# Performance work log

Measured on AMD Instinct MI355X. Metric: run time of the kernel, lower is better.

The kernel has to match this reference:

```python
import jax, jax.numpy as jnp
import numpy as np

POS_TH = 0.5
NEG_TH = 0.4
NEGPOS_RATIO = 3
BBOX_ALPHA = 1.5
CONF_ALPHA = 1.0
VAR_CXCY = 0.1
VAR_WH = 0.2
NUM_CLASSES = 41
B, P, G = 8, 100000, 16


def setup_inputs() -> dict:
    key = jax.random.key(0)
    k = jax.random.split(key, 8)
    loc_data = jax.random.normal(k[0], (B, P, 4), dtype=jnp.float32)
    conf_data = jax.random.normal(k[1], (B, P, NUM_CLASSES), dtype=jnp.float32)
    # priors in (cx, cy, w, h), normalized coords
    p_cxy = jax.random.uniform(k[2], (P, 2), minval=0.0, maxval=1.0)
    p_wh = jax.random.uniform(k[3], (P, 2), minval=0.02, maxval=0.3)
    priors = jnp.concatenate([p_cxy, p_wh], axis=1).astype(jnp.float32)
    # gt boxes in point form (x1, y1, x2, y2)
    g_cxy = jax.random.uniform(k[4], (B, G, 2), minval=0.15, maxval=0.85)
    g_wh = jax.random.uniform(k[5], (B, G, 2), minval=0.05, maxval=0.4)
    gt_boxes = jnp.concatenate([
        jnp.clip(g_cxy - g_wh / 2, 0.0, 1.0),
        jnp.clip(g_cxy + g_wh / 2, 0.0, 1.0),
    ], axis=-1).astype(jnp.float32)
    gt_labels = jax.random.randint(k[6], (B, G), 1, NUM_CLASSES)
    return {"loc_data": loc_data, "conf_data": conf_data, "priors": priors,
            "gt_boxes": gt_boxes, "gt_labels": gt_labels}


def point_form(pr):
    return jnp.concatenate([pr[:, :2] - pr[:, 2:] / 2,
                            pr[:, :2] + pr[:, 2:] / 2], axis=1)


def jaccard(a, b):
    # a: [G,4] xyxy, b: [P,4] xyxy -> [G,P]
    lt = jnp.maximum(a[:, None, :2], b[None, :, :2])
    rb = jnp.minimum(a[:, None, 2:], b[None, :, 2:])
    wh = jnp.clip(rb - lt, 0.0)
    inter = wh[..., 0] * wh[..., 1]
    area_a = ((a[:, 2] - a[:, 0]) * (a[:, 3] - a[:, 1]))[:, None]
    area_b = ((b[:, 2] - b[:, 0]) * (b[:, 3] - b[:, 1]))[None, :]
    return inter / (area_a + area_b - inter)


def encode(matched, priors):
    # matched [P,4] xyxy, priors [P,4] cxcywh -> SSD offsets with variances
    g_cxcy = ((matched[:, :2] + matched[:, 2:]) / 2 - priors[:, :2]) / (VAR_CXCY * priors[:, 2:])
    g_wh = jnp.log(jnp.clip((matched[:, 2:] - matched[:, :2]) / priors[:, 2:], 1e-8)) / VAR_WH
    return jnp.concatenate([g_cxcy, g_wh], axis=1)


def match_one(gt_box, gt_label, priors):
    # gt_box [G,4], gt_label [G], priors [P,4] -> loc_t [P,4], conf_t [P]
    pf = point_form(priors)
    ov = jaccard(gt_box, pf)                      # [G,P]
    best_truth_ov = ov.max(axis=0)                # [P]
    best_truth_idx = ov.argmax(axis=0)            # [P]
    best_prior_idx = ov.argmax(axis=1)            # [G] best prior per gt
    # force-match each gt to its best prior
    best_truth_ov = best_truth_ov.at[best_prior_idx].set(2.0)
    best_truth_idx = best_truth_idx.at[best_prior_idx].set(jnp.arange(gt_box.shape[0]))
    conf = gt_label[best_truth_idx]
    conf = jnp.where(best_truth_ov < POS_TH, -1, conf)   # neutral
    conf = jnp.where(best_truth_ov < NEG_TH, 0, conf)    # background
    loc = encode(gt_box[best_truth_idx], priors)
    return loc, conf


def reference(loc_data, conf_data, priors, gt_boxes, gt_labels):
    bsz, n_pri, n_cls = conf_data.shape
    loc_t, conf_t = jax.vmap(match_one, in_axes=(0, 0, None))(gt_boxes, gt_labels, priors)
    pos = conf_t > 0                               # [B,P]
    num_pos = pos.sum(axis=1)                      # [B]
    # pos_weights: uniform 1/num_pos per image (ones split then normalized)
    pos_w = pos.astype(loc_data.dtype) / jnp.clip(num_pos, 1).astype(loc_data.dtype)[:, None]
    # localization: weighted SmoothL1 over positives
    d = loc_data - loc_t
    sl1 = jnp.where(jnp.abs(d) < 1.0, 0.5 * d * d, jnp.abs(d) - 0.5)
    loss_B = (pos_w[..., None] * sl1).sum() * BBOX_ALPHA
    # OHEM hard negative mining on background-suppression loss
    loss_c = jax.nn.logsumexp(conf_data, axis=-1) - conf_data[..., 0]
    loss_c = jnp.where(pos | (conf_t < 0), 0.0, loss_c)
    order = jnp.argsort(-loss_c, axis=1)
    rank = jnp.argsort(order, axis=1)
    num_neg = jnp.clip(NEGPOS_RATIO * num_pos, 0, n_pri - 1)
    neg = (rank < num_neg[:, None]) & (~pos) & (conf_t >= 0)
    keep = (pos | neg).astype(conf_data.dtype)
    logp = jax.nn.log_softmax(conf_data, axis=-1)
    ce = -jnp.take_along_axis(logp, jnp.clip(conf_t, 0)[..., None], axis=-1)[..., 0]
    total_pos = jnp.clip(num_pos.sum(), 1).astype(conf_data.dtype)
    loss_C = (ce * keep).sum() * CONF_ALPHA / total_pos
    return (loss_B + loss_C) / bsz
```

## Files before the change

### kernel.cpp

```cpp
#include <hip/hip_runtime.h>
#include <stdint.h>

#define BATCH 8
#define NPRI 100000
#define NGT 16
#define NCLS 41
#define F_POS_TH 0.5f
#define F_NEG_TH 0.4f

static constexpr int TPB = 256;
static constexpr int PBLK = (NPRI + TPB - 1) / TPB;
static constexpr int HBLK = 64;
static constexpr int NBIN = 4096;

static constexpr size_t OFF_KEY  = 0;
static constexpr size_t OFF_CE   = OFF_KEY + (size_t)BATCH*NPRI*8;
static constexpr size_t OFF_CT   = OFF_CE  + (size_t)BATCH*NPRI*4;
static constexpr size_t OFF_OV   = OFF_CT  + (size_t)BATCH*NPRI*4;
static constexpr size_t OFF_BTI  = OFF_OV  + (size_t)BATCH*NPRI*4;
static constexpr size_t OFF_GTC  = OFF_BTI + (size_t)BATCH*NPRI*4;
static constexpr size_t OFF_ZERO = OFF_GTC + BATCH*NGT*8;
static constexpr size_t OFF_HIST = OFF_ZERO;
static constexpr size_t OFF_PREF = OFF_HIST + (size_t)4*BATCH*NBIN*4;
static constexpr size_t OFF_KREM = OFF_PREF + BATCH*8;
static constexpr size_t OFF_NPOS = OFF_KREM + BATCH*4;
static constexpr size_t OFF_SL1  = OFF_NPOS + BATCH*4;
static constexpr size_t OFF_CES  = OFF_SL1  + BATCH*4;
static constexpr size_t ZERO_BYTES = OFF_CES + BATCH*4 - OFF_ZERO;

__device__ inline float smoothl1(float d) {
  float a = fabsf(d);
  return a < 1.f ? 0.5f * d * d : a - 0.5f;
}

__global__ void k_init(unsigned long long* __restrict__ gtc) {
  int i = threadIdx.x;
  if (i < BATCH * NGT) gtc[i] = 0xFFFFFFFFull;
}

__global__ __launch_bounds__(TPB) void k_match(const float* __restrict__ priors,
                                               const float* __restrict__ gtb,
                                               float* __restrict__ ov_out,
                                               int* __restrict__ bti_out,
                                               unsigned long long* __restrict__ gtc) {
  int b = blockIdx.y;
  int t = threadIdx.x;
  int p = blockIdx.x * TPB + t;
  __shared__ unsigned long long best[NGT];
  if (t < NGT) best[t] = 0;
  __syncthreads();
  bool valid = p < NPRI;
  int pc = valid ? p : 0;
  const float4 pv = ((const float4*)priors)[pc];
  float px1 = pv.x - 0.5f * pv.z, py1 = pv.y - 0.5f * pv.w;
  float px2 = pv.x + 0.5f * pv.z, py2 = pv.y + 0.5f * pv.w;
  float parea = (px2 - px1) * (py2 - py1);
  float bov = 0.f; int bidx = 0;
#pragma unroll
  for (int g = 0; g < NGT; g++) {
    const float4 gv = ((const float4*)gtb)[b * NGT + g];
    float ix = fmaxf(fminf(px2, gv.z) - fmaxf(px1, gv.x), 0.f);
    float iy = fmaxf(fminf(py2, gv.w) - fmaxf(py1, gv.y), 0.f);
    float inter = ix * iy;
    float garea = (gv.z - gv.x) * (gv.w - gv.y);
    float iou = inter / (parea + garea - inter);
    if (!valid) iou = 0.f;
    if (iou > bov) { bov = iou; bidx = g; }
    if (iou > 0.f) {
      unsigned long long comp = ((unsigned long long)__float_as_uint(iou) << 32)
                              | (unsigned long long)(0xFFFFFFFFu - (unsigned)p);
      if (comp > best[g]) atomicMax(&best[g], comp);
    }
  }
  if (valid) {
    ov_out[b * NPRI + p] = bov;
    bti_out[b * NPRI + p] = bidx;
  }
  __syncthreads();
  if (t < NGT && best[t] != 0) atomicMax(&gtc[b * NGT + t], best[t]);
}

__global__ __launch_bounds__(TPB) void k_conf(
    const float* __restrict__ loc, const float* __restrict__ conf,
    const float* __restrict__ priors, const float* __restrict__ gtb,
    const int* __restrict__ gtl, const unsigned long long* __restrict__ gtc,
    const float* __restrict__ ov, const int* __restrict__ bti,
    unsigned long long* __restrict__ key, float* __restrict__ ce,
    int* __restrict__ ct, unsigned* __restrict__ npos, float* __restrict__ sl1sum) {
  __shared__ float rows[TPB * NCLS];
  __shared__ float red_s[4];
  __shared__ unsigned red_p[4];
  int b = blockIdx.y;
  int p0 = blockIdx.x * TPB;
  int t = threadIdx.x;
  int nrows = min(TPB, NPRI - p0);
  int n4 = nrows * NCLS / 4;
  const float4* src4 = (const float4*)(conf + ((size_t)b * NPRI + p0) * NCLS);
  float4* rows4 = (float4*)rows;
  if (nrows == TPB) {
    float4 tmp[10];
#pragma unroll
    for (int u = 0; u < 10; u++) tmp[u] = src4[t + u * TPB];
    float4 extra = src4[10 * TPB + t];
#pragma unroll
    for (int u = 0; u < 10; u++) rows4[t + u * TPB] = tmp[u];
    if (t < n4 - 10 * TPB) rows4[10 * TPB + t] = extra;
  } else {
    for (int i = t; i < n4; i += TPB) rows4[i] = src4[i];
  }
  __syncthreads();
  int p = p0 + t;
  bool valid = p < NPRI;
  float my_sl1 = 0.f;
  unsigned my_pos = 0;
  if (valid) {
    float o = ov[b * NPRI + p];
    int g = bti[b * NPRI + p];
#pragma unroll
    for (int gg = 0; gg < NGT; gg++) {
      unsigned long long c64 = gtc[b * NGT + gg];
      unsigned pw = 0xFFFFFFFFu - (unsigned)(c64 & 0xFFFFFFFFull);
      if ((unsigned)p == pw) { o = 2.0f; g = gg; }
    }
    int c = gtl[b * NGT + g];
    if (o < F_POS_TH) c = -1;
    if (o < F_NEG_TH) c = 0;
    ct[b * NPRI + p] = c;
    const float* r = rows + t * NCLS;
    float s = 0.f;
#pragma unroll
    for (int j = 0; j < NCLS; j++) s += __expf(r[j]);
    float lse = __logf(s);
    int tgt = c > 0 ? c : 0;
    ce[b * NPRI + p] = lse - r[tgt];
    float lc = (c == 0) ? (lse - r[0]) : 0.f;
    key[b * NPRI + p] = ((unsigned long long)__float_as_uint(lc) << 17)
                      | (unsigned long long)(0x1FFFFu - (unsigned)p);
    if (c > 0) {
      my_pos = 1;
      const float4 pv = ((const float4*)priors)[p];
      const float4 gv = ((const float4*)gtb)[b * NGT + g];
      float tx = ((gv.x + gv.z) * 0.5f - pv.x) / (0.1f * pv.z);
      float ty = ((gv.y + gv.w) * 0.5f - pv.y) / (0.1f * pv.w);
      float tw = __logf(fmaxf((gv.z - gv.x) / pv.z, 1e-8f)) / 0.2f;
      float th = __logf(fmaxf((gv.w - gv.y) / pv.w, 1e-8f)) / 0.2f;
      const float4 ld = ((const float4*)loc)[(size_t)b * NPRI + p];
      my_sl1 = smoothl1(ld.x - tx) + smoothl1(ld.y - ty)
             + smoothl1(ld.z - tw) + smoothl1(ld.w - th);
    }
  }
  float vs = my_sl1; unsigned vp = my_pos;
#pragma unroll
  for (int off = 32; off; off >>= 1) {
    vs += __shfl_down(vs, off, 64);
    vp += __shfl_down(vp, off, 64);
  }
  if ((t & 63) == 0) { red_s[t >> 6] = vs; red_p[t >> 6] = vp; }
  __syncthreads();
  if (t == 0) {
    float ts = red_s[0] + red_s[1] + red_s[2] + red_s[3];
    unsigned tp = red_p[0] + red_p[1] + red_p[2] + red_p[3];
    if (tp) atomicAdd(&npos[b], tp);
    if (ts != 0.f) atomicAdd(&sl1sum[b], ts);
  }
}

__global__ __launch_bounds__(TPB) void k_histp(const unsigned long long* __restrict__ key,
                                               unsigned* __restrict__ hist,
                                               const unsigned long long* __restrict__ prefix,
                                               int shift) {
  __shared__ unsigned h[NBIN];
  int b = blockIdx.y;
  int t = threadIdx.x;
  for (int i = t; i < NBIN; i += TPB) h[i] = 0;
  __syncthreads();
  unsigned long long pre = prefix[b] >> (shift + 12);
  for (int i = blockIdx.x * TPB + t; i < NPRI; i += HBLK * TPB) {
    unsigned long long k = key[b * NPRI + i];
    if ((k >> (shift + 12)) == pre)
      atomicAdd(&h[(unsigned)((k >> shift) & 0xFFFull)], 1u);
  }
  __syncthreads();
  for (int i = t; i < NBIN; i += TPB) {
    unsigned v = h[i];
    if (v) atomicAdd(&hist[((size_t)b << 12) + i], v);
  }
}

__global__ __launch_bounds__(256) void k_fine(const unsigned* __restrict__ hist,
                                              unsigned long long* __restrict__ prefix,
                                              unsigned* __restrict__ krem,
                                              const unsigned* __restrict__ npos,
                                              int shift, int pass) {
  int b = blockIdx.x;
  int t = threadIdx.x;
  __shared__ unsigned part[256];
  __shared__ unsigned suf[256];
  __shared__ int wA;
  __shared__ unsigned kexclA;
  unsigned k = (pass == 0) ? min(3u * npos[b], (unsigned)(NPRI - 1)) : krem[b];
  if (k == 0) {
    if (t == 0) prefix[b] = ~0ull;
    return;
  }
  const unsigned* h = hist + ((size_t)b << 12);
  unsigned s = 0;
#pragma unroll
  for (int u = 0; u < 16; u++) s += h[t * 16 + u];
  part[t] = s; suf[t] = s;
  __syncthreads();
  for (int off = 1; off < 256; off <<= 1) {
    unsigned v = (t + off < 256) ? suf[t + off] : 0;
    __syncthreads();
    suf[t] += v;
    __syncthreads();
  }
  unsigned excl = suf[t] - part[t];
  if (excl < k && k <= excl + part[t]) { wA = t; kexclA = excl; }
  __syncthreads();
  int w = wA;
  unsigned exclw = kexclA;
  if (t < 64) {
    unsigned v = (t < 16) ? h[w * 16 + t] : 0;
    unsigned sufv = v;
#pragma unroll
    for (int off = 1; off < 16; off <<= 1) {
      unsigned x = __shfl_down(sufv, off, 64);
      if (t + off < 16) sufv += x;
    }
    unsigned excl2 = exclw + (sufv - v);
    if (t < 16 && excl2 < k && k <= excl2 + v) {
      unsigned digit = (unsigned)(w * 16 + t);
      prefix[b] |= ((unsigned long long)digit) << shift;
      krem[b] = k - excl2;
    }
  }
}

__global__ __launch_bounds__(TPB) void k_eval(const unsigned long long* __restrict__ key,
                                              const float* __restrict__ ce,
                                              const int* __restrict__ ct,
                                              const unsigned long long* __restrict__ prefix,
                                              float* __restrict__ cesum) {
  __shared__ float red[4];
  int b = blockIdx.y;
  int t = threadIdx.x;
  int p = blockIdx.x * TPB + t;
  float v = 0.f;
  if (p < NPRI) {
    int c = ct[b * NPRI + p];
    bool keep = (c > 0) || (c == 0 && key[b * NPRI + p] >= prefix[b]);
    if (keep) v = ce[b * NPRI + p];
  }
#pragma unroll
  for (int off = 32; off; off >>= 1) v += __shfl_down(v, off, 64);
  if ((t & 63) == 0) red[t >> 6] = v;
  __syncthreads();
  if (t == 0) {
    float tv = red[0] + red[1] + red[2] + red[3];
    if (tv != 0.f) atomicAdd(&cesum[b], tv);
  }
}

__global__ void k_final(const float* __restrict__ sl1sum, const unsigned* __restrict__ npos,
                        const float* __restrict__ cesum, float* __restrict__ out) {
  if (threadIdx.x == 0 && blockIdx.x == 0) {
    float lb = 0.f, cs = 0.f;
    unsigned tp = 0;
    for (int b = 0; b < BATCH; b++) {
      lb += sl1sum[b] / fmaxf((float)npos[b], 1.f);
      tp += npos[b];
      cs += cesum[b];
    }
    float lc = cs / fmaxf((float)tp, 1.f);
    out[0] = (1.5f * lb + 1.0f * lc) / (float)BATCH;
  }
}

extern "C" void kernel_launch(void* const* d_in, const int* in_sizes, int n_in,
                              void* d_out, int out_size, void* d_ws, size_t ws_size,
                              hipStream_t stream) {
  const float* loc = (const float*)d_in[0];
  const float* conf = (const float*)d_in[1];
  const float* priors = (const float*)d_in[2];
  const float* gtb = (const float*)d_in[3];
  const int* gtl = (const int*)d_in[4];
  char* ws = (char*)d_ws;
  unsigned long long* key = (unsigned long long*)(ws + OFF_KEY);
  float* ce = (float*)(ws + OFF_CE);
  int* ct = (int*)(ws + OFF_CT);
  float* ov = (float*)(ws + OFF_OV);
  int* bti = (int*)(ws + OFF_BTI);
  unsigned long long* gtc = (unsigned long long*)(ws + OFF_GTC);
  unsigned* hist = (unsigned*)(ws + OFF_HIST);
  unsigned long long* prefix = (unsigned long long*)(ws + OFF_PREF);
  unsigned* krem = (unsigned*)(ws + OFF_KREM);
  unsigned* npos = (unsigned*)(ws + OFF_NPOS);
  float* sl1sum = (float*)(ws + OFF_SL1);
  float* cesum = (float*)(ws + OFF_CES);
  float* out = (float*)d_out;

  hipMemsetAsync(ws + OFF_ZERO, 0, ZERO_BYTES, stream);
  k_init<<<1, 128, 0, stream>>>(gtc);
  dim3 gridP(PBLK, BATCH);
  k_match<<<gridP, TPB, 0, stream>>>(priors, gtb, ov, bti, gtc);
  k_conf<<<gridP, TPB, 0, stream>>>(loc, conf, priors, gtb, gtl, gtc, ov, bti,
                                    key, ce, ct, npos, sl1sum);
  dim3 gridH(HBLK, BATCH);
  const int shifts[4] = {36, 24, 12, 0};
  for (int pass = 0; pass < 4; pass++) {
    unsigned* h = hist + (size_t)pass * BATCH * NBIN;
    k_histp<<<gridH, TPB, 0, stream>>>(key, h, prefix, shifts[pass]);
    k_fine<<<BATCH, 256, 0, stream>>>(h, prefix, krem, npos, shifts[pass], pass);
  }
  k_eval<<<gridP, TPB, 0, stream>>>(key, ce, ct, prefix, cesum);
  k_final<<<1, 64, 0, stream>>>(sl1sum, npos, cesum, out);
}
```

Before: 182.0 us.

## Fuse radix-select histogram and scan via last-block ticket, sum negatives from histograms

Merges the per-pass histogram and prefix-select kernels into one kernel. The last block to finish, detected with an atomic ticket, performs the scan and resets the global histograms. Each bin now also accumulates the sum of its keys' loss values, so the hard-negative CE sum comes straight from the histograms and the separate eval pass plus the ce/ct buffers go away. The final reduction moves into the last pass, and k_conf now reads conf rows directly per thread rather than staging them through shared memory. The trade-offs are float-atomic summation order, a ticket-based cross-block sync, uncoalesced strided row reads in k_conf, and a tie at the threshold handled by proportional averaging.

After: 344.2 us. 89.1% more time.

```diff
diff --git a/kernel.cpp b/kernel.cpp
--- a/kernel.cpp
+++ b/kernel.cpp
@@ -14,28 +14,42 @@
 static constexpr int NBIN = 4096;
 
 static constexpr size_t OFF_KEY  = 0;
-static constexpr size_t OFF_CE   = OFF_KEY + (size_t)BATCH*NPRI*8;
-static constexpr size_t OFF_CT   = OFF_CE  + (size_t)BATCH*NPRI*4;
-static constexpr size_t OFF_OV   = OFF_CT  + (size_t)BATCH*NPRI*4;
+static constexpr size_t OFF_OV   = OFF_KEY + (size_t)BATCH*NPRI*8;
 static constexpr size_t OFF_BTI  = OFF_OV  + (size_t)BATCH*NPRI*4;
 static constexpr size_t OFF_GTC  = OFF_BTI + (size_t)BATCH*NPRI*4;
 static constexpr size_t OFF_ZERO = OFF_GTC + BATCH*NGT*8;
-static constexpr size_t OFF_HIST = OFF_ZERO;
-static constexpr size_t OFF_PREF = OFF_HIST + (size_t)4*BATCH*NBIN*4;
-static constexpr size_t OFF_KREM = OFF_PREF + BATCH*8;
+static constexpr size_t OFF_HC   = OFF_ZERO;
+static constexpr size_t OFF_HS   = OFF_HC + (size_t)BATCH*NBIN*4;
+static constexpr size_t OFF_PREF = OFF_HS + (size_t)BATCH*NBIN*4;
+static constexpr size_t OFF_TK   = OFF_PREF + BATCH*8;
+static constexpr size_t OFF_KREM = OFF_TK   + BATCH*4;
 static constexpr size_t OFF_NPOS = OFF_KREM + BATCH*4;
 static constexpr size_t OFF_SL1  = OFF_NPOS + BATCH*4;
-static constexpr size_t OFF_CES  = OFF_SL1  + BATCH*4;
-static constexpr size_t ZERO_BYTES = OFF_CES + BATCH*4 - OFF_ZERO;
+static constexpr size_t OFF_CEP  = OFF_SL1  + BATCH*4;
+static constexpr size_t OFF_NEG  = OFF_CEP  + BATCH*4;
+static constexpr size_t OFF_FTK  = OFF_NEG  + BATCH*4;
+static constexpr size_t OFF_END  = OFF_FTK + 4;
+static constexpr size_t ZERO_BYTES = OFF_END - OFF_ZERO;
+static_assert(ZERO_BYTES % 4 == 0, "zero region u32-granular");
 
 __device__ inline float smoothl1(float d) {
   float a = fabsf(d);
   return a < 1.f ? 0.5f * d * d : a - 0.5f;
 }
 
-__global__ void k_init(unsigned long long* __restrict__ gtc) {
-  int i = threadIdx.x;
-  if (i < BATCH * NGT) gtc[i] = 0xFFFFFFFFull;
+__device__ inline unsigned aload_u32(const unsigned* p) {
+  return __hip_atomic_load(p, __ATOMIC_RELAXED, __HIP_MEMORY_SCOPE_AGENT);
+}
+__device__ inline float aload_f32(const float* p) {
+  return __hip_atomic_load(p, __ATOMIC_RELAXED, __HIP_MEMORY_SCOPE_AGENT);
+}
+
+__global__ void k_init(unsigned* __restrict__ z, unsigned long long* __restrict__ gtc) {
+  const int n = (int)(ZERO_BYTES / 4);
+  for (int i = blockIdx.x * blockDim.x + threadIdx.x; i < n; i += gridDim.x * blockDim.x)
+    z[i] = 0u;
+  if (blockIdx.x == 0 && threadIdx.x < BATCH * NGT)
+    gtc[threadIdx.x] = 0xFFFFFFFFull;
 }
 
 __global__ __launch_bounds__(TPB) void k_match(const float* __restrict__ priors,
@@ -85,35 +99,15 @@
     const float* __restrict__ priors, const float* __restrict__ gtb,
     const int* __restrict__ gtl, const unsigned long long* __restrict__ gtc,
     const float* __restrict__ ov, const int* __restrict__ bti,
-    unsigned long long* __restrict__ key, float* __restrict__ ce,
-    int* __restrict__ ct, unsigned* __restrict__ npos, float* __restrict__ sl1sum) {
-  __shared__ float rows[TPB * NCLS];
-  __shared__ float red_s[4];
-  __shared__ unsigned red_p[4];
+    unsigned long long* __restrict__ key,
+    unsigned* __restrict__ npos, float* __restrict__ sl1sum, float* __restrict__ cepos) {
+  __shared__ float red_s[4]; __shared__ unsigned red_p[4]; __shared__ float red_c[4];
   int b = blockIdx.y;
-  int p0 = blockIdx.x * TPB;
   int t = threadIdx.x;
-  int nrows = min(TPB, NPRI - p0);
-  int n4 = nrows * NCLS / 4;
-  const float4* src4 = (const float4*)(conf + ((size_t)b * NPRI + p0) * NCLS);
-  float4* rows4 = (float4*)rows;
-  if (nrows == TPB) {
-    float4 tmp[10];
-#pragma unroll
-    for (int u = 0; u < 10; u++) tmp[u] = src4[t + u * TPB];
-    float4 extra = src4[10 * TPB + t];
-#pragma unroll
-    for (int u = 0; u < 10; u++) rows4[t + u * TPB] = tmp[u];
-    if (t < n4 - 10 * TPB) rows4[10 * TPB + t] = extra;
-  } else {
-    for (int i = t; i < n4; i += TPB) rows4[i] = src4[i];
-  }
-  __syncthreads();
-  int p = p0 + t;
-  bool valid = p < NPRI;
-  float my_sl1 = 0.f;
+  int p = blockIdx.x * TPB + t;
+  float my_sl1 = 0.f, my_ce = 0.f;
   unsigned my_pos = 0;
-  if (valid) {
+  if (p < NPRI) {
     float o = ov[b * NPRI + p];
     int g = bti[b * NPRI + p];
 #pragma unroll
@@ -125,19 +119,22 @@
     int c = gtl[b * NGT + g];
     if (o < F_POS_TH) c = -1;
     if (o < F_NEG_TH) c = 0;
-    ct[b * NPRI + p] = c;
-    const float* r = rows + t * NCLS;
-    float s = 0.f;
-#pragma unroll
-    for (int j = 0; j < NCLS; j++) s += __expf(r[j]);
+    const float* row = conf + ((size_t)b * NPRI + p) * NCLS;
+    float s = 0.f, r0 = 0.f, rc = 0.f;
+#pragma unroll
+    for (int j = 0; j < NCLS; j++) {
+      float v = row[j];
+      s += __expf(v);
+      if (j == 0) r0 = v;
+      if (j == c) rc = v;
+    }
     float lse = __logf(s);
-    int tgt = c > 0 ? c : 0;
-    ce[b * NPRI + p] = lse - r[tgt];
-    float lc = (c == 0) ? (lse - r[0]) : 0.f;
-    key[b * NPRI + p] = ((unsigned long long)__float_as_uint(lc) << 17)
-                      | (unsigned long long)(0x1FFFFu - (unsigned)p);
+    float lc = (c == 0) ? (lse - r0) : 0.f;
+    key[(size_t)b * NPRI + p] = ((unsigned long long)__float_as_uint(lc) << 17)
+                              | (unsigned long long)(0x1FFFFu - (unsigned)p);
     if (c > 0) {
       my_pos = 1;
+      my_ce = lse - rc;
       const float4 pv = ((const float4*)priors)[p];
       const float4 gv = ((const float4*)gtb)[b * NGT + g];
       float tx = ((gv.x + gv.z) * 0.5f - pv.x) / (0.1f * pv.z);
@@ -149,131 +146,131 @@
              + smoothl1(ld.z - tw) + smoothl1(ld.w - th);
     }
   }
-  float vs = my_sl1; unsigned vp = my_pos;
+  float vs = my_sl1, vc = my_ce; unsigned vp = my_pos;
 #pragma unroll
   for (int off = 32; off; off >>= 1) {
     vs += __shfl_down(vs, off, 64);
+    vc += __shfl_down(vc, off, 64);
     vp += __shfl_down(vp, off, 64);
   }
-  if ((t & 63) == 0) { red_s[t >> 6] = vs; red_p[t >> 6] = vp; }
+  if ((t & 63) == 0) { red_s[t >> 6] = vs; red_c[t >> 6] = vc; red_p[t >> 6] = vp; }
   __syncthreads();
   if (t == 0) {
     float ts = red_s[0] + red_s[1] + red_s[2] + red_s[3];
+    float tc = red_c[0] + red_c[1] + red_c[2] + red_c[3];
     unsigned tp = red_p[0] + red_p[1] + red_p[2] + red_p[3];
     if (tp) atomicAdd(&npos[b], tp);
     if (ts != 0.f) atomicAdd(&sl1sum[b], ts);
-  }
-}
-
-__global__ __launch_bounds__(TPB) void k_histp(const unsigned long long* __restrict__ key,
-                                               unsigned* __restrict__ hist,
-                                               const unsigned long long* __restrict__ prefix,
-                                               int shift) {
-  __shared__ unsigned h[NBIN];
+    if (tc != 0.f) atomicAdd(&cepos[b], tc);
+  }
+}
+
+__global__ __launch_bounds__(256) void k_histfine(
+    const unsigned long long* __restrict__ key,
+    unsigned* __restrict__ hc_g, float* __restrict__ hs_g,
+    unsigned* __restrict__ ticket, unsigned long long* __restrict__ prefix,
+    unsigned* __restrict__ krem, const unsigned* __restrict__ npos,
+    float* __restrict__ negsum, const float* __restrict__ sl1sum,
+    const float* __restrict__ cepos, unsigned* __restrict__ final_tk,
+    float* __restrict__ out, int shift, int pass) {
+  __shared__ unsigned hc[NBIN];
+  __shared__ float hs[NBIN];
+  __shared__ unsigned pc[256]; __shared__ float ps[256];
+  __shared__ unsigned sc[256]; __shared__ float ss[256];
+  __shared__ int wA; __shared__ unsigned kexA; __shared__ float aboveA;
+  __shared__ unsigned rk;
   int b = blockIdx.y;
   int t = threadIdx.x;
-  for (int i = t; i < NBIN; i += TPB) h[i] = 0;
+  for (int i = t; i < NBIN; i += 256) { hc[i] = 0; hs[i] = 0.f; }
   __syncthreads();
   unsigned long long pre = prefix[b] >> (shift + 12);
-  for (int i = blockIdx.x * TPB + t; i < NPRI; i += HBLK * TPB) {
-    unsigned long long k = key[b * NPRI + i];
-    if ((k >> (shift + 12)) == pre)
-      atomicAdd(&h[(unsigned)((k >> shift) & 0xFFFull)], 1u);
-  }
-  __syncthreads();
-  for (int i = t; i < NBIN; i += TPB) {
-    unsigned v = h[i];
-    if (v) atomicAdd(&hist[((size_t)b << 12) + i], v);
-  }
-}
-
-__global__ __launch_bounds__(256) void k_fine(const unsigned* __restrict__ hist,
-                                              unsigned long long* __restrict__ prefix,
-                                              unsigned* __restrict__ krem,
-                                              const unsigned* __restrict__ npos,
-                                              int shift, int pass) {
-  int b = blockIdx.x;
-  int t = threadIdx.x;
-  __shared__ unsigned part[256];
-  __shared__ unsigned suf[256];
-  __shared__ int wA;
-  __shared__ unsigned kexclA;
+  for (int i = blockIdx.x * 256 + t; i < NPRI; i += HBLK * 256) {
+    unsigned long long kk = key[(size_t)b * NPRI + i];
+    if ((kk >> (shift + 12)) == pre) {
+      unsigned d = (unsigned)((kk >> shift) & 0xFFFull);
+      atomicAdd(&hc[d], 1u);
+      atomicAdd(&hs[d], __uint_as_float((unsigned)(kk >> 17)));
+    }
+  }
+  __syncthreads();
+  unsigned base = ((unsigned)b) << 12;
+  for (int i = t; i < NBIN; i += 256) {
+    unsigned c = hc[i]; if (c) atomicAdd(&hc_g[base + i], c);
+    float sv = hs[i];   if (sv != 0.f) atomicAdd(&hs_g[base + i], sv);
+  }
+  __threadfence();
+  if (t == 0) rk = atomicAdd(&ticket[b], 1u);
+  __syncthreads();
+  if (rk != HBLK - 1) return;
+  __threadfence();
   unsigned k = (pass == 0) ? min(3u * npos[b], (unsigned)(NPRI - 1)) : krem[b];
-  if (k == 0) {
-    if (t == 0) prefix[b] = ~0ull;
-    return;
-  }
-  const unsigned* h = hist + ((size_t)b << 12);
-  unsigned s = 0;
-#pragma unroll
-  for (int u = 0; u < 16; u++) s += h[t * 16 + u];
-  part[t] = s; suf[t] = s;
+  for (int i = t; i < NBIN; i += 256) {
+    hc[i] = aload_u32(&hc_g[base + i]);
+    hs[i] = aload_f32(&hs_g[base + i]);
+    hc_g[base + i] = 0u;
+    hs_g[base + i] = 0.f;
+  }
+  if (t == 0) { ticket[b] = 0; wA = -1; }
+  __syncthreads();
+  unsigned cs = 0; float fs = 0.f;
+#pragma unroll
+  for (int u = 0; u < 16; u++) { cs += hc[t * 16 + u]; fs += hs[t * 16 + u]; }
+  pc[t] = cs; sc[t] = cs; ps[t] = fs; ss[t] = fs;
   __syncthreads();
   for (int off = 1; off < 256; off <<= 1) {
-    unsigned v = (t + off < 256) ? suf[t + off] : 0;
+    unsigned v = (t + off < 256) ? sc[t + off] : 0;
+    float fv = (t + off < 256) ? ss[t + off] : 0.f;
     __syncthreads();
-    suf[t] += v;
+    sc[t] += v; ss[t] += fv;
     __syncthreads();
   }
-  unsigned excl = suf[t] - part[t];
-  if (excl < k && k <= excl + part[t]) { wA = t; kexclA = excl; }
-  __syncthreads();
-  int w = wA;
-  unsigned exclw = kexclA;
-  if (t < 64) {
-    unsigned v = (t < 16) ? h[w * 16 + t] : 0;
-    unsigned sufv = v;
+  unsigned excl = sc[t] - pc[t];
+  if (k > 0 && excl < k && k <= excl + pc[t]) {
+    wA = t; kexA = excl; aboveA = ss[t] - ps[t];
+  }
+  __syncthreads();
+  if (wA >= 0 && t < 64) {
+    int w = wA; unsigned exw = kexA;
+    unsigned v = (t < 16) ? hc[w * 16 + t] : 0;
+    float fv = (t < 16) ? hs[w * 16 + t] : 0.f;
+    unsigned sufv = v; float suff = fv;
 #pragma unroll
     for (int off = 1; off < 16; off <<= 1) {
       unsigned x = __shfl_down(sufv, off, 64);
-      if (t + off < 16) sufv += x;
-    }
-    unsigned excl2 = exclw + (sufv - v);
+      float xf = __shfl_down(suff, off, 64);
+      if (t + off < 16) { sufv += x; suff += xf; }
+    }
+    unsigned excl2 = exw + (sufv - v);
     if (t < 16 && excl2 < k && k <= excl2 + v) {
-      unsigned digit = (unsigned)(w * 16 + t);
-      prefix[b] |= ((unsigned long long)digit) << shift;
-      krem[b] = k - excl2;
-    }
-  }
-}
-
-__global__ __launch_bounds__(TPB) void k_eval(const unsigned long long* __restrict__ key,
-                                              const float* __restrict__ ce,
-                                              const int* __restrict__ ct,
-                                              const unsigned long long* __restrict__ prefix,
-                                              float* __restrict__ cesum) {
-  __shared__ float red[4];
-  int b = blockIdx.y;
-  int t = threadIdx.x;
-  int p = blockIdx.x * TPB + t;
-  float v = 0.f;
-  if (p < NPRI) {
-    int c = ct[b * NPRI + p];
-    bool keep = (c > 0) || (c == 0 && key[b * NPRI + p] >= prefix[b]);
-    if (keep) v = ce[b * NPRI + p];
-  }
-#pragma unroll
-  for (int off = 32; off; off >>= 1) v += __shfl_down(v, off, 64);
-  if ((t & 63) == 0) red[t >> 6] = v;
-  __syncthreads();
-  if (t == 0) {
-    float tv = red[0] + red[1] + red[2] + red[3];
-    if (tv != 0.f) atomicAdd(&cesum[b], tv);
-  }
-}
-
-__global__ void k_final(const float* __restrict__ sl1sum, const unsigned* __restrict__ npos,
-                        const float* __restrict__ cesum, float* __restrict__ out) {
-  if (threadIdx.x == 0 && blockIdx.x == 0) {
-    float lb = 0.f, cs = 0.f;
-    unsigned tp = 0;
-    for (int b = 0; b < BATCH; b++) {
-      lb += sl1sum[b] / fmaxf((float)npos[b], 1.f);
-      tp += npos[b];
-      cs += cesum[b];
-    }
-    float lc = cs / fmaxf((float)tp, 1.f);
-    out[0] = (1.5f * lb + 1.0f * lc) / (float)BATCH;
+      float contrib = aboveA + (suff - fv);
+      if (pass == 3) {
+        contrib += fv * ((float)(k - excl2) / (float)v);
+      } else {
+        prefix[b] |= ((unsigned long long)(w * 16 + t)) << shift;
+        krem[b] = k - excl2;
+      }
+      if (contrib != 0.f) atomicAdd(&negsum[b], contrib);
+    }
+  }
+  if (pass == 3) {
+    __syncthreads();
+    if (t == 0) {
+      __threadfence();
+      unsigned r2 = atomicAdd(final_tk, 1u);
+      if (r2 == BATCH - 1) {
+        __threadfence();
+        float lb = 0.f, ctot = 0.f;
+        unsigned tp = 0;
+        for (int bb = 0; bb < BATCH; bb++) {
+          float ns = aload_f32(&negsum[bb]);
+          lb += sl1sum[bb] / fmaxf((float)npos[bb], 1.f);
+          tp += npos[bb];
+          ctot += cepos[bb] + ns;
+        }
+        out[0] = (1.5f * lb + ctot / fmaxf((float)tp, 1.f)) / (float)BATCH;
+        *final_tk = 0;
+      }
+    }
   }
 }
 
@@ -287,32 +284,31 @@
   const int* gtl = (const int*)d_in[4];
   char* ws = (char*)d_ws;
   unsigned long long* key = (unsigned long long*)(ws + OFF_KEY);
-  float* ce = (float*)(ws + OFF_CE);
-  int* ct = (int*)(ws + OFF_CT);
   float* ov = (float*)(ws + OFF_OV);
   int* bti = (int*)(ws + OFF_BTI);
   unsigned long long* gtc = (unsigned long long*)(ws + OFF_GTC);
-  unsigned* hist = (unsigned*)(ws + OFF_HIST);
+  unsigned* hc_g = (unsigned*)(ws + OFF_HC);
+  float* hs_g = (float*)(ws + OFF_HS);
   unsigned long long* prefix = (unsigned long long*)(ws + OFF_PREF);
+  unsigned* ticket = (unsigned*)(ws + OFF_TK);
   unsigned* krem = (unsigned*)(ws + OFF_KREM);
   unsigned* npos = (unsigned*)(ws + OFF_NPOS);
   float* sl1sum = (float*)(ws + OFF_SL1);
-  float* cesum = (float*)(ws + OFF_CES);
+  float* cepos = (float*)(ws + OFF_CEP);
+  float* negsum = (float*)(ws + OFF_NEG);
+  unsigned* final_tk = (unsigned*)(ws + OFF_FTK);
   float* out = (float*)d_out;
 
-  hipMemsetAsync(ws + OFF_ZERO, 0, ZERO_BYTES, stream);
-  k_init<<<1, 128, 0, stream>>>(gtc);
+  k_init<<<64, TPB, 0, stream>>>((unsigned*)(ws + OFF_ZERO), gtc);
   dim3 gridP(PBLK, BATCH);
   k_match<<<gridP, TPB, 0, stream>>>(priors, gtb, ov, bti, gtc);
   k_conf<<<gridP, TPB, 0, stream>>>(loc, conf, priors, gtb, gtl, gtc, ov, bti,
-                                    key, ce, ct, npos, sl1sum);
+                                    key, npos, sl1sum, cepos);
   dim3 gridH(HBLK, BATCH);
   const int shifts[4] = {36, 24, 12, 0};
   for (int pass = 0; pass < 4; pass++) {
-    unsigned* h = hist + (size_t)pass * BATCH * NBIN;
-    k_histp<<<gridH, TPB, 0, stream>>>(key, h, prefix, shifts[pass]);
-    k_fine<<<BATCH, 256, 0, stream>>>(h, prefix, krem, npos, shifts[pass], pass);
-  }
-  k_eval<<<gridP, TPB, 0, stream>>>(key, ce, ct, prefix, cesum);
-  k_final<<<1, 64, 0, stream>>>(sl1sum, npos, cesum, out);
-}
+    k_histfine<<<gridH, 256, 0, stream>>>(key, hc_g, hs_g, ticket, prefix, krem,
+                                          npos, negsum, sl1sum, cepos, final_tk,
+                                          out, shifts[pass], pass);
+  }
+}
```
